# Optimization experiments

Measured on AMD Instinct MI355X. Metric: run time of the kernel, lower is better.

Reference implementation:

```python
import jax, jax.numpy as jnp
import numpy as np

DIM = 1024
SEQ_LEN = 4096
K = 256
HEADS = 16
DIM_HEAD = DIM // HEADS  # 64
BATCH = 4


def setup_inputs() -> dict:
    key = jax.random.key(0)
    ks = jax.random.split(key, 8)
    x = jax.random.normal(ks[0], (BATCH, SEQ_LEN, DIM), dtype=jnp.float32)
    # nn.Linear weights are [out, in]; y = x @ W.T
    std_lin = 1.0 / np.sqrt(DIM)
    Wq = jax.random.uniform(ks[1], (HEADS * DIM_HEAD, DIM), minval=-std_lin, maxval=std_lin, dtype=jnp.float32)
    Wk = jax.random.uniform(ks[2], (HEADS * DIM_HEAD, DIM), minval=-std_lin, maxval=std_lin, dtype=jnp.float32)
    Wv = jax.random.uniform(ks[3], (HEADS * DIM_HEAD, DIM), minval=-std_lin, maxval=std_lin, dtype=jnp.float32)
    # proj_k/proj_v init_: uniform(-1/sqrt(k), 1/sqrt(k)) on [seq_len, k]
    std_p = 1.0 / np.sqrt(K)
    proj_k = jax.random.uniform(ks[4], (SEQ_LEN, K), minval=-std_p, maxval=std_p, dtype=jnp.float32)
    proj_v = jax.random.uniform(ks[5], (SEQ_LEN, K), minval=-std_p, maxval=std_p, dtype=jnp.float32)
    std_o = 1.0 / np.sqrt(HEADS * DIM_HEAD)
    Wo = jax.random.uniform(ks[6], (DIM, HEADS * DIM_HEAD), minval=-std_o, maxval=std_o, dtype=jnp.float32)
    bo = jax.random.uniform(ks[7], (DIM,), minval=-std_o, maxval=std_o, dtype=jnp.float32)
    return {"x": x, "Wq": Wq, "Wk": Wk, "Wv": Wv, "proj_k": proj_k, "proj_v": proj_v, "Wo": Wo, "bo": bo}


def reference(x, Wq, Wk, Wv, proj_k, proj_v, Wo, bo):
    b, n, d = x.shape
    h, dh, k = HEADS, DIM_HEAD, K
    # q/k/v projections
    q = jnp.einsum('bnd,ed->bne', x, Wq)            # [b, n, h*dh]
    keys = jnp.einsum('bnd,ed->bne', x, Wk)         # [b, n, h*dh]
    vals = jnp.einsum('bnd,ed->bne', x, Wv)         # [b, n, h*dh]
    # low-rank projection along sequence: [b, n, e] x [n, k] -> [b, k, e]
    keys = jnp.einsum('bne,nk->bke', keys, proj_k[:n])
    vals = jnp.einsum('bne,nk->bke', vals, proj_v[:n])
    # split heads
    q = q.reshape(b, n, h, dh).transpose(0, 2, 1, 3)        # [b, h, n, dh]
    keys = keys.reshape(b, k, h, dh).transpose(0, 2, 1, 3)  # [b, h, k, dh]
    vals = vals.reshape(b, k, h, dh).transpose(0, 2, 1, 3)  # [b, h, k, dh]
    dots = jnp.einsum('bhnd,bhkd->bhnk', q, keys) * (dh ** -0.5)
    attn = jax.nn.softmax(dots, axis=-1)
    out = jnp.einsum('bhnk,bhkd->bhnd', attn, vals)
    out = out.transpose(0, 2, 1, 3).reshape(b, n, h * dh)
    return jnp.einsum('bne,oe->bno', out, Wo) + bo
```

## Files before the change

kernel.cpp:

```cpp
#include <hip/hip_runtime.h>
#include <hip/hip_bf16.h>
#include <stdint.h>

typedef unsigned short u16;
typedef __attribute__((ext_vector_type(8))) short bf16x8;
typedef __attribute__((ext_vector_type(4))) float f32x4;

#define DEV __device__ __forceinline__

DEV u16 f2bf(float f) {
  union { float f; unsigned u; } v; v.f = f;
  unsigned r = (v.u + 0x7fffu + ((v.u >> 16) & 1u)) >> 16;
  return (u16)r;
}

DEV unsigned pk2(float lo, float hi) {
  union { __hip_bfloat162 h; unsigned u; } c;
  c.h = __float22bfloat162_rn(make_float2(lo, hi));
  return c.u;
}

DEV f32x4 mfma16(bf16x8 a, bf16x8 b, f32x4 c) {
  return __builtin_amdgcn_mfma_f32_16x16x32_bf16(a, b, c, 0, 0, 0);
}

DEV void gload_lds16(const u16* g, u16* l) {
  __builtin_amdgcn_global_load_lds((const __attribute__((address_space(1))) void*)g,
                                   (__attribute__((address_space(3))) void*)l, 16, 0, 0);
}

#define QSCALE 0.18033688011112042f

__global__ void cvt_xpose_kernel(const float* __restrict__ src, u16* __restrict__ dst_rm,
                                 u16* __restrict__ dst_tp, int R, int C,
                                 long zS, long zRM, long zTP) {
  __shared__ u16 tile[64][72];
  src += (size_t)blockIdx.z * zS;
  dst_tp += (size_t)blockIdx.z * zTP;
  int r0 = blockIdx.y * 64, c0 = blockIdx.x * 64;
  int tr = threadIdx.x >> 2, tc = (threadIdx.x & 3) * 16;
  const float* s = src + (size_t)(r0 + tr) * C + c0 + tc;
  u16 loc[16];
#pragma unroll
  for (int q = 0; q < 4; ++q) {
    float4 v = ((const float4*)s)[q];
    loc[q * 4 + 0] = f2bf(v.x); loc[q * 4 + 1] = f2bf(v.y);
    loc[q * 4 + 2] = f2bf(v.z); loc[q * 4 + 3] = f2bf(v.w);
  }
#pragma unroll
  for (int i = 0; i < 16; ++i) tile[tr][tc + i] = loc[i];
  if (dst_rm) {
    u16* d = dst_rm + (size_t)blockIdx.z * zRM + (size_t)(r0 + tr) * C + c0 + tc;
    *(bf16x8*)d = *(const bf16x8*)&loc[0];
    *(bf16x8*)(d + 8) = *(const bf16x8*)&loc[8];
  }
  __syncthreads();
  u16 tmp[16];
#pragma unroll
  for (int i = 0; i < 16; ++i) tmp[i] = tile[tc + i][tr];
  u16* d = dst_tp + (size_t)(c0 + tr) * R + r0 + tc;
  *(bf16x8*)d = *(const bf16x8*)&tmp[0];
  *(bf16x8*)(d + 8) = *(const bf16x8*)&tmp[8];
}

__global__ void cvt_w4_kernel(const float* __restrict__ s0, const float* __restrict__ s1,
                              const float* __restrict__ s2, const float* __restrict__ s3,
                              u16* __restrict__ d0, u16* __restrict__ d1,
                              u16* __restrict__ d2, u16* __restrict__ d3) {
  const float* s; u16* d;
  switch (blockIdx.y) {
    case 0: s = s0; d = d0; break;
    case 1: s = s1; d = d1; break;
    case 2: s = s2; d = d2; break;
    default: s = s3; d = d3; break;
  }
  int i = blockIdx.x * 256 + threadIdx.x;
  float4 v = ((const float4*)s)[i];
  ushort4 o; o.x = f2bf(v.x); o.y = f2bf(v.y); o.z = f2bf(v.z); o.w = f2bf(v.w);
  ((ushort4*)d)[i] = o;
}

__global__ void reduce4_kernel(const float* __restrict__ part, u16* __restrict__ out) {
  int i = blockIdx.x * 256 + threadIdx.x;
  const float4* p = (const float4*)part;
  float4 a = p[i], b = p[i + 524288], c = p[i + 1048576], d = p[i + 1572864];
  ushort4 o;
  o.x = f2bf(a.x + b.x + c.x + d.x);
  o.y = f2bf(a.y + b.y + c.y + d.y);
  o.z = f2bf(a.z + b.z + c.z + d.z);
  o.w = f2bf(a.w + b.w + c.w + d.w);
  ((ushort4*)out)[i] = o;
}

template<int OMODE>
__global__ __launch_bounds__(256, 4)
void gemm_bt_kernel(const u16* __restrict__ A, const u16* __restrict__ Bt,
                    const u16* __restrict__ Bt2, void* __restrict__ Cout,
                    u16* __restrict__ CoutT, const float* __restrict__ bias, float cscale,
                    int ldA, int ldB, int ldC, int Klen,
                    long zA, long zB, long zC, int bMod, long kChunk) {
  __shared__ __align__(16) u16 smA[2][128 * 32];
  __shared__ __align__(16) u16 smB[2][128 * 32];
  const int t = threadIdx.x;
  const int lane = t & 63, wave = t >> 6;
  const int wm = wave & 1, wn = wave >> 1;
  const int g = lane >> 4, r = lane & 15;
  const int id = (blockIdx.y << 3) | blockIdx.x;
  const int s = (id & 7) * gridDim.y + (id >> 3);
  const int bx = s & 7, by = s >> 3;
  const int z = blockIdx.z;
  const int b = z % bMod, kc = z / bMod;
  const u16* Ab = A + (size_t)b * zA + (size_t)kc * kChunk;
  const u16* Bbase = (Bt2 && (b & 1)) ? Bt2 : Bt;
  const u16* Bb = Bbase + (size_t)b * zB + (size_t)kc * kChunk;
  const int m0 = by * 128, n0 = bx * 128;
  const int srow = t >> 2;
  const int lslot = ((t & 3) + 4 - ((srow >> 1) & 3)) & 3;

  f32x4 acc[4][4];
#pragma unroll
  for (int m = 0; m < 4; ++m)
#pragma unroll
    for (int n = 0; n < 4; ++n) acc[m][n] = f32x4{0.f, 0.f, 0.f, 0.f};

  auto STAGE = [&](int buf, int k0) {
#pragma unroll
    for (int p = 0; p < 2; ++p) {
      int row = p * 64 + srow;
      gload_lds16(Ab + (size_t)(m0 + row) * ldA + k0 + lslot * 8, &smA[buf][p * 2048 + wave * 512]);
      gload_lds16(Bb + (size_t)(n0 + row) * ldB + k0 + lslot * 8, &smB[buf][p * 2048 + wave * 512]);
    }
  };

  const int nt = Klen >> 5;
  STAGE(0, 0);
  __syncthreads();
  int cur = 0;
  for (int it = 0; it < nt; ++it) {
    if (it + 1 < nt) STAGE(cur ^ 1, (it + 1) << 5);
    bf16x8 af[4], bfr[4];
#pragma unroll
    for (int m = 0; m < 4; ++m) {
      int row = wm * 64 + m * 16 + r;
      int ps = (g + (row >> 1)) & 3;
      af[m] = *(const bf16x8*)&smA[cur][row * 32 + ps * 8];
    }
#pragma unroll
    for (int n = 0; n < 4; ++n) {
      int row = wn * 64 + n * 16 + r;
      int ps = (g + (row >> 1)) & 3;
      bfr[n] = *(const bf16x8*)&smB[cur][row * 32 + ps * 8];
    }
#pragma unroll
    for (int m = 0; m < 4; ++m)
#pragma unroll
      for (int n = 0; n < 4; ++n)
        acc[m][n] = mfma16(af[m], bfr[n], acc[m][n]);
    __syncthreads();
    cur ^= 1;
  }

  if constexpr (OMODE == 0) {
    u16* C = (u16*)Cout + (size_t)z * zC;
#pragma unroll
    for (int n = 0; n < 4; ++n) {
      int col = n0 + wn * 64 + n * 16 + r;
#pragma unroll
      for (int m = 0; m < 4; ++m) {
        int rowb = m0 + wm * 64 + m * 16 + 4 * g;
#pragma unroll
        for (int rr = 0; rr < 4; ++rr)
          C[(size_t)(rowb + rr) * ldC + col] = f2bf(acc[m][n][rr] * cscale);
      }
    }
  } else if constexpr (OMODE == 3) {
    if ((z & 1) == 0) {
      u16* C = (u16*)Cout + (size_t)(z >> 1) * zC;
#pragma unroll
      for (int n = 0; n < 4; ++n) {
        int col = n0 + wn * 64 + n * 16 + r;
#pragma unroll
        for (int m = 0; m < 4; ++m) {
          int rowb = m0 + wm * 64 + m * 16 + 4 * g;
#pragma unroll
          for (int rr = 0; rr < 4; ++rr)
            C[(size_t)(rowb + rr) * ldC + col] = f2bf(acc[m][n][rr]);
        }
      }
    } else {
      u16* C = CoutT + (size_t)(z >> 1) * zC;
#pragma unroll
      for (int n = 0; n < 4; ++n) {
        int col = n0 + wn * 64 + n * 16 + r;
#pragma unroll
        for (int m = 0; m < 4; ++m) {
          int rowb = m0 + wm * 64 + m * 16 + 4 * g;
          ushort4 o;
          o.x = f2bf(acc[m][n][0]); o.y = f2bf(acc[m][n][1]);
          o.z = f2bf(acc[m][n][2]); o.w = f2bf(acc[m][n][3]);
          *(ushort4*)&C[(size_t)col * 256 + rowb] = o;
        }
      }
    }
  } else {
    float* C = (float*)Cout + (size_t)z * zC;
#pragma unroll
    for (int n = 0; n < 4; ++n) {
      int col = n0 + wn * 64 + n * 16 + r;
      float bv = (OMODE == 1) ? bias[col] : 0.f;
#pragma unroll
      for (int m = 0; m < 4; ++m) {
        int rowb = m0 + wm * 64 + m * 16 + 4 * g;
#pragma unroll
        for (int rr = 0; rr < 4; ++rr)
          C[(size_t)(rowb + rr) * ldC + col] = acc[m][n][rr] + bv;
      }
    }
  }
}

#define MFMA_CLUSTER(MH, NH, AF, BV)                                                    \
  do {                                                                                  \
    __builtin_amdgcn_s_barrier();                                                       \
    __builtin_amdgcn_sched_barrier(0);                                                  \
    __builtin_amdgcn_s_setprio(1);                                                      \
    _Pragma("unroll")                                                                   \
    for (int mi = 0; mi < 4; ++mi)                                                      \
      _Pragma("unroll")                                                                 \
      for (int ni = 0; ni < 2; ++ni) {                                                  \
        acc[(MH)*4+mi][(NH)*2+ni] = mfma16(AF[mi][0], BV[ni][0], acc[(MH)*4+mi][(NH)*2+ni]); \
        acc[(MH)*4+mi][(NH)*2+ni] = mfma16(AF[mi][1], BV[ni][1], acc[(MH)*4+mi][(NH)*2+ni]); \
      }                                                                                 \
    __builtin_amdgcn_s_setprio(0);                                                      \
  } while (0)

#define ENDBAR(W)                                                                       \
  do {                                                                                  \
    if ((W) == 1) asm volatile("s_waitcnt vmcnt(4)" ::: "memory");                      \
    if ((W) == 2) asm volatile("s_waitcnt vmcnt(0)" ::: "memory");                      \
    __builtin_amdgcn_s_barrier();                                                       \
    __builtin_amdgcn_sched_barrier(0);                                                  \
  } while (0)

template<int OMODE>
__global__ __launch_bounds__(512, 1)
void gemm256_kernel(const u16* __restrict__ A, const u16* __restrict__ Bt,
                    void* __restrict__ Cout, const float* __restrict__ bias,
                    float cscale, int ldA, int ldB, int ldC, int Klen) {
  __shared__ __align__(16) u16 lds[65536];
  const int t = threadIdx.x;
  const int lane = t & 63, wave = t >> 6;
  const int g = lane >> 4, r = lane & 15, rm = r & 7;
  const int wm = wave >> 2, wn = wave & 3;
  const int id = blockIdx.y * 4 + blockIdx.x;
  const int sw = (id & 7) * 32 + (id >> 3);
  const int bx = sw & 3, by = sw >> 2;
  const int m0 = by * 256, n0 = bx * 256;

  const int trow = t >> 3, tslot = t & 7;
  const int sslot = tslot ^ (trow & 7);
  const u16* Asrc = A + (size_t)(m0 + trow) * ldA + sslot * 8;
  const u16* Bsrc = Bt + sslot * 8;
  const int bRow0 = n0 + (trow >> 5) * 64 + (trow & 31);
  const int bRow1 = n0 + (2 + (trow >> 5)) * 64 + (trow & 31);

  u16* const A0 = lds;
  u16* const A1 = lds + 16384;
  u16* const B0 = lds + 32768;
  u16* const B1 = lds + 49152;

  auto stageA = [&](u16* buf, int h, int k0) {
    u16* d = buf + h * 8192 + t * 8;
    const u16* s0 = Asrc + (size_t)(h * 64) * ldA + k0;
    gload_lds16(s0, d);
    gload_lds16(s0 + (size_t)128 * ldA, d + 4096);
  };
  auto stageB = [&](u16* buf, int h, int k0) {
    u16* d = buf + h * 8192 + t * 8;
    gload_lds16(Bsrc + (size_t)(bRow0 + h * 32) * ldB + k0, d);
    gload_lds16(Bsrc + (size_t)(bRow1 + h * 32) * ldB + k0, d + 4096);
  };

  const int aoff = wm * 64 + r;
  const int boff = wn * 32 + r;

  auto loadA = [&](bf16x8 af[4][2], const u16* base, int MH) {
#pragma unroll
    for (int mi = 0; mi < 4; ++mi) {
      const u16* rp = base + (MH * 128 + aoff + mi * 16) * 64;
      af[mi][0] = *(const bf16x8*)&rp[(g ^ rm) * 8];
      af[mi][1] = *(const bf16x8*)&rp[((4 + g) ^ rm) * 8];
    }
  };
  auto loadB = [&](bf16x8 bv[2][2], const u16* base, int NH) {
#pragma unroll
    for (int ni = 0; ni < 2; ++ni) {
      const u16* rp = base + (NH * 128 + boff + ni * 16) * 64;
      bv[ni][0] = *(const bf16x8*)&rp[(g ^ rm) * 8];
      bv[ni][1] = *(const bf16x8*)&rp[((4 + g) ^ rm) * 8];
    }
  };

  f32x4 acc[8][4];
#pragma unroll
  for (int m = 0; m < 8; ++m)
#pragma unroll
    for (int n = 0; n < 4; ++n) acc[m][n] = f32x4{0.f, 0.f, 0.f, 0.f};

  stageA(A0, 0, 0); stageB(B0, 0, 0); stageA(A0, 1, 0); stageB(B0, 1, 0);
  stageA(A1, 0, 64); stageB(B1, 0, 64);
  asm volatile("s_waitcnt vmcnt(4)" ::: "memory");
  __builtin_amdgcn_s_barrier();
  __builtin_amdgcn_sched_barrier(0);

  const int nt = Klen >> 6;
  for (int j = 0; j < (nt >> 1); ++j) {
    const int ta = 2 * j, tb = ta + 1;
    const int more = (ta + 2 < nt);
    const int kb = tb * 64, kn = (ta + 2) * 64, kn2 = (tb + 2) * 64;
    bf16x8 af[4][2], bv0[2][2], bv1[2][2];
    loadA(af, A0, 0); loadB(bv0, B0, 0);
    stageA(A1, 1, kb);
    MFMA_CLUSTER(0, 0, af, bv0); ENDBAR(0);
    loadB(bv1, B0, 1);
    stageB(B1, 1, kb);
    MFMA_CLUSTER(0, 1, af, bv1); ENDBAR(0);
    loadA(af, A0, 1);
    if (more) stageA(A0, 0, kn);
    MFMA_CLUSTER(1, 0, af, bv0); ENDBAR(0);
    if (more) stageB(B0, 0, kn);
    MFMA_CLUSTER(1, 1, af, bv1); ENDBAR(more ? 1 : 2);
    loadA(af, A1, 0); loadB(bv0, B1, 0);
    if (more) stageA(A0, 1, kn);
    MFMA_CLUSTER(0, 0, af, bv0); ENDBAR(0);
    loadB(bv1, B1, 1);
    if (more) stageB(B0, 1, kn);
    MFMA_CLUSTER(0, 1, af, bv1); ENDBAR(0);
    loadA(af, A1, 1);
    if (more) stageA(A1, 0, kn2);
    MFMA_CLUSTER(1, 0, af, bv0); ENDBAR(0);
    if (more) stageB(B1, 0, kn2);
    MFMA_CLUSTER(1, 1, af, bv1); ENDBAR(more ? 1 : 2);
  }

  if constexpr (OMODE == 0) {
    u16* myT = lds + wave * 8192;
#pragma unroll
    for (int m = 0; m < 8; ++m)
#pragma unroll
      for (int n = 0; n < 4; ++n)
#pragma unroll
        for (int rr = 0; rr < 4; ++rr) {
          int rl = m * 16 + 4 * g + rr;
          int cl = n * 16 + r;
          myT[rl * 64 + (((cl >> 3) ^ (rl & 7)) << 3) + (cl & 7)] = f2bf(acc[m][n][rr] * cscale);
        }
    u16* Cg = (u16*)Cout + (size_t)(m0 + wm * 128) * ldC + n0 + wn * 64;
#pragma unroll
    for (int i = 0; i < 16; ++i) {
      int idx = i * 64 + lane;
      int row = idx >> 3, c8 = idx & 7;
      bf16x8 v = *(const bf16x8*)&myT[row * 64 + ((c8 ^ (row & 7)) << 3)];
      *(bf16x8*)&Cg[(size_t)row * ldC + c8 * 8] = v;
    }
  } else {
    float* myF = (float*)lds + wave * 4096;
    float bvn[4];
#pragma unroll
    for (int n = 0; n < 4; ++n) bvn[n] = bias[n0 + wn * 64 + n * 16 + r];
    float* Cg = (float*)Cout + (size_t)(m0 + wm * 128) * ldC + n0 + wn * 64;
#pragma unroll
    for (int half = 0; half < 2; ++half) {
#pragma unroll
      for (int m2 = 0; m2 < 4; ++m2)
#pragma unroll
        for (int n = 0; n < 4; ++n)
#pragma unroll
          for (int rr = 0; rr < 4; ++rr) {
            int rl = m2 * 16 + 4 * g + rr;
            int cl = n * 16 + r;
            myF[rl * 64 + (((cl >> 2) ^ (rl & 15)) << 2) + (cl & 3)] =
                acc[half * 4 + m2][n][rr] + bvn[n];
          }
#pragma unroll
      for (int i = 0; i < 16; ++i) {
        int idx = i * 64 + lane;
        int row = idx >> 4, c4 = idx & 15;
        float4 v = *(const float4*)&myF[row * 64 + ((c4 ^ (row & 15)) << 2)];
        *(float4*)&Cg[(size_t)(half * 64 + row) * ldC + c4 * 4] = v;
      }
    }
  }
}

__global__ __launch_bounds__(256, 4)
void attn_kernel(const u16* __restrict__ Q, const u16* __restrict__ Kl,
                 const u16* __restrict__ VT, u16* __restrict__ Out) {
  __shared__ __align__(16) u16 sm[20480];
  const int t = threadIdx.x, lane = t & 63, w = t >> 6;
  const int g = lane >> 4, r = lane & 15;
  const int id = (blockIdx.y << 6) | blockIdx.x;
  const int s = (id & 7) * (gridDim.y << 3) + (id >> 3);
  const int b = blockIdx.z, h = s >> 6, n0 = (s & 63) * 64;
  const u16* Kb = Kl + (size_t)b * 262144 + h * 64;
  const u16* Vb = VT + (size_t)b * 262144 + (size_t)(h * 64) * 256;
  u16* vbase = sm + 16384;

  const int vd = t >> 2;
  const int vsl = (t & 3) ^ (vd & 3);
  auto stage_slice = [&](int kk, int buf) {
    gload_lds16(Vb + (size_t)vd * 256 + kk * 32 + vsl * 8, vbase + buf * 2048 + w * 512);
  };

#pragma unroll
  for (int p = 0; p < 8; ++p) {
    int row = p * 32 + (t >> 3);
    int ls = ((t & 7) + 8 - (row & 7)) & 7;
    gload_lds16(Kb + (size_t)row * 1024 + ls * 8, sm + p * 2048 + w * 512);
  }
  stage_slice(0, 0);
  stage_slice(1, 1);
  const int qrow = n0 + w * 16 + r;
  const u16* Qp = Q + ((size_t)(b * 4096 + qrow)) * 1024 + h * 64 + g * 8;
  bf16x8 aq0 = *(const bf16x8*)Qp;
  bf16x8 aq1 = *(const bf16x8*)(Qp + 32);
  __syncthreads();

  f32x4 dotv[16];
  __builtin_amdgcn_s_setprio(1);
#pragma unroll
  for (int kf = 0; kf < 16; ++kf) {
    int row = kf * 16 + r;
    bf16x8 kb0 = *(const bf16x8*)&sm[row * 64 + ((g + row) & 7) * 8];
    bf16x8 kb1 = *(const bf16x8*)&sm[row * 64 + ((4 + g + row) & 7) * 8];
    f32x4 d = f32x4{0.f, 0.f, 0.f, 0.f};
    d = mfma16(kb0, aq0, d);
    d = mfma16(kb1, aq1, d);
    dotv[kf] = d;
  }
  __builtin_amdgcn_s_setprio(0);
  __syncthreads();

  float mx = -3.4e38f;
#pragma unroll
  for (int kf = 0; kf < 16; ++kf)
    mx = fmaxf(mx, fmaxf(fmaxf(dotv[kf][0], dotv[kf][1]), fmaxf(dotv[kf][2], dotv[kf][3])));
  mx = fmaxf(mx, __shfl_xor(mx, 16, 64));
  mx = fmaxf(mx, __shfl_xor(mx, 32, 64));
  float ssum = 0.f;
#pragma unroll
  for (int kf = 0; kf < 16; ++kf)
#pragma unroll
    for (int j = 0; j < 4; ++j) {
      float p = __builtin_amdgcn_exp2f(dotv[kf][j] - mx);
      dotv[kf][j] = p;
      ssum += p;
    }
  ssum += __shfl_xor(ssum, 16, 64);
  ssum += __shfl_xor(ssum, 32, 64);
  const float inv = 1.f / ssum;
  float invv[4];
#pragma unroll
  for (int rr = 0; rr < 4; ++rr) invv[rr] = __shfl(inv, 4 * g + rr, 64);

  const int q16 = w * 16 + r;
  const int qx = (q16 & 7) << 3;
#pragma unroll
  for (int kf = 0; kf < 16; ++kf) {
    uint2 val;
    val.x = pk2(dotv[kf][0], dotv[kf][1]);
    val.y = pk2(dotv[kf][2], dotv[kf][3]);
    *(uint2*)&sm[(q16 * 256 + kf * 16 + 4 * g) ^ qx] = val;
  }

  f32x4 oacc[4];
#pragma unroll
  for (int df = 0; df < 4; ++df) oacc[df] = f32x4{0.f, 0.f, 0.f, 0.f};
#pragma unroll
  for (int kk = 0; kk < 8; ++kk) {
    bf16x8 ap = *(const bf16x8*)&sm[(q16 * 256 + kk * 32 + g * 8) ^ qx];
    const u16* vb = vbase + (kk & 1) * 2048;
    __builtin_amdgcn_s_setprio(1);
#pragma unroll
    for (int df = 0; df < 4; ++df) {
      int d = df * 16 + r;
      bf16x8 bv = *(const bf16x8*)&vb[d * 32 + (g ^ (d & 3)) * 8];
      oacc[df] = mfma16(ap, bv, oacc[df]);
    }
    __builtin_amdgcn_s_setprio(0);
    if (kk < 7) {
      __syncthreads();
      if (kk < 6) stage_slice(kk + 2, kk & 1);
    }
  }

  u16* myO = sm + w * 4096;
#pragma unroll
  for (int df = 0; df < 4; ++df)
#pragma unroll
    for (int rr = 0; rr < 4; ++rr) {
      int row = 4 * g + rr;
      int col = df * 16 + r;
      myO[row * 64 + (((col >> 3) ^ (row & 7)) << 3) + (col & 7)] = f2bf(oacc[df][rr] * invv[rr]);
    }
#pragma unroll
  for (int i = 0; i < 2; ++i) {
    int idx = i * 64 + lane;
    int row = idx >> 3, c8 = idx & 7;
    bf16x8 v = *(const bf16x8*)&myO[row * 64 + ((c8 ^ (row & 7)) << 3)];
    *(bf16x8*)&Out[((size_t)(b * 4096 + n0 + w * 16 + row)) * 1024 + h * 64 + c8 * 8] = v;
  }
}

extern "C" void kernel_launch(void* const* d_in, const int* in_sizes, int n_in,
                              void* d_out, int out_size, void* d_ws, size_t ws_size,
                              hipStream_t stream) {
  const float* x  = (const float*)d_in[0];
  const float* Wq = (const float*)d_in[1];
  const float* Wk = (const float*)d_in[2];
  const float* Wv = (const float*)d_in[3];
  const float* pk = (const float*)d_in[4];
  const float* pv = (const float*)d_in[5];
  const float* Wo = (const float*)d_in[6];
  const float* bo = (const float*)d_in[7];

  u16* ws = (u16*)d_ws;
  u16* xbf   = ws;
  u16* xT    = xbf + 16777216;
  u16* wqb   = xT + 16777216;
  u16* wkb   = wqb + 1048576;
  u16* wvb   = wkb + 1048576;
  u16* wob   = wvb + 1048576;
  u16* projT = wob + 1048576;
  u16* Qb    = projT + 2097152;
  u16* xp    = Qb + 16777216;
  u16* klow  = xp + 2097152;
  u16* vT    = klow + 1048576;
  u16* aout  = xbf;
  float* xp_part = (float*)Qb;

  cvt_xpose_kernel<<<dim3(16, 64, 4), 256, 0, stream>>>(x, xbf, xT, 4096, 1024,
                                                        4194304, 4194304, 4194304);
  cvt_w4_kernel<<<dim3(1024, 4), 256, 0, stream>>>(Wq, Wk, Wv, Wo, wqb, wkb, wvb, wob);
  cvt_xpose_kernel<<<dim3(4, 64, 1), 256, 0, stream>>>(pk, nullptr, projT, 4096, 256, 0, 0, 0);
  cvt_xpose_kernel<<<dim3(4, 64, 1), 256, 0, stream>>>(pv, nullptr, projT + 1048576, 4096, 256, 0, 0, 0);
  gemm_bt_kernel<2><<<dim3(8, 4, 16), 256, 0, stream>>>(
      projT, xT, nullptr, (void*)xp_part, nullptr, nullptr, 1.f,
      4096, 4096, 1024, 1024, 0, 4194304, 524288, 4, 1024);
  reduce4_kernel<<<2048, 256, 0, stream>>>(xp_part, xp);
  gemm_bt_kernel<3><<<dim3(8, 2, 8), 256, 0, stream>>>(
      xp, wkb, wvb, (void*)klow, vT, nullptr, 1.f,
      1024, 1024, 1024, 1024, 262144, 0, 262144, 8, 0);
  gemm256_kernel<0><<<dim3(4, 64), 512, 0, stream>>>(
      xbf, wqb, (void*)Qb, nullptr, QSCALE, 1024, 1024, 1024, 1024);
  attn_kernel<<<dim3(64, 16, 4), 256, 0, stream>>>(Qb, klow, vT, aout);
  gemm256_kernel<1><<<dim3(4, 64), 512, 0, stream>>>(
      aout, wob, d_out, bo, 1.f, 1024, 1024, 1024, 1024);
}
```

Baseline: 211.7 us.

## Batch-merge projT×xT GEMM, add LDS-staged coalesced fp32 split-K output, trim barriers

```diff
diff --git a/kernel.cpp b/kernel.cpp
--- a/kernel.cpp
+++ b/kernel.cpp
@@ -98,21 +98,22 @@
                     const u16* __restrict__ Bt2, void* __restrict__ Cout,
                     u16* __restrict__ CoutT, const float* __restrict__ bias, float cscale,
                     int ldA, int ldB, int ldC, int Klen,
-                    long zA, long zB, long zC, int bMod, long kChunk) {
+                    long zA, long zB, long zC, int bMod, long kChunkA, long kChunkB) {
   __shared__ __align__(16) u16 smA[2][128 * 32];
   __shared__ __align__(16) u16 smB[2][128 * 32];
   const int t = threadIdx.x;
   const int lane = t & 63, wave = t >> 6;
   const int wm = wave & 1, wn = wave >> 1;
   const int g = lane >> 4, r = lane & 15;
-  const int id = (blockIdx.y << 3) | blockIdx.x;
-  const int s = (id & 7) * gridDim.y + (id >> 3);
-  const int bx = s & 7, by = s >> 3;
+  const int id = blockIdx.y * gridDim.x + blockIdx.x;
+  const int cpx = (gridDim.x * gridDim.y) >> 3;
+  const int s = (id & 7) * cpx + (id >> 3);
+  const int bx = s % gridDim.x, by = s / gridDim.x;
   const int z = blockIdx.z;
   const int b = z % bMod, kc = z / bMod;
-  const u16* Ab = A + (size_t)b * zA + (size_t)kc * kChunk;
+  const u16* Ab = A + (size_t)b * zA + (size_t)kc * kChunkA;
   const u16* Bbase = (Bt2 && (b & 1)) ? Bt2 : Bt;
-  const u16* Bb = Bbase + (size_t)b * zB + (size_t)kc * kChunk;
+  const u16* Bb = Bbase + (size_t)b * zB + (size_t)kc * kChunkB;
   const int m0 = by * 128, n0 = bx * 128;
   const int srow = t >> 2;
   const int lslot = ((t & 3) + 4 - ((srow >> 1) & 3)) & 3;
@@ -172,6 +173,32 @@
         for (int rr = 0; rr < 4; ++rr)
           C[(size_t)(rowb + rr) * ldC + col] = f2bf(acc[m][n][rr] * cscale);
       }
+    }
+  } else if constexpr (OMODE == 2) {
+    float* myF = ((float*)(wave < 2 ? (void*)&smA[0][0] : (void*)&smB[0][0])) + (wave & 1) * 2048;
+    float* Cg = (float*)Cout + (size_t)z * zC + (size_t)(m0 + wm * 64) * ldC + n0 + wn * 64;
+#pragma unroll
+    for (int np = 0; np < 2; ++np) {
+#pragma unroll
+      for (int n2 = 0; n2 < 2; ++n2)
+#pragma unroll
+        for (int m = 0; m < 4; ++m)
+#pragma unroll
+          for (int rr = 0; rr < 4; ++rr) {
+            int rl = m * 16 + 4 * g + rr;
+            int cl = n2 * 16 + r;
+            myF[rl * 32 + ((((cl >> 2) ^ (rl & 7)) & 7) << 2) + (cl & 3)] =
+                acc[m][np * 2 + n2][rr];
+          }
+      __syncthreads();
+#pragma unroll
+      for (int i = 0; i < 8; ++i) {
+        int idx = i * 64 + lane;
+        int row = idx >> 3, c = idx & 7;
+        float4 v = *(const float4*)&myF[row * 32 + (((c ^ (row & 7)) & 7) << 2)];
+        *(float4*)&Cg[(size_t)row * ldC + np * 32 + c * 4] = v;
+      }
+      __syncthreads();
     }
   } else if constexpr (OMODE == 3) {
     if ((z & 1) == 0) {
@@ -221,8 +248,6 @@
 
 #define MFMA_CLUSTER(MH, NH, AF, BV)                                                    \
   do {                                                                                  \
-    __builtin_amdgcn_s_barrier();                                                       \
-    __builtin_amdgcn_sched_barrier(0);                                                  \
     __builtin_amdgcn_s_setprio(1);                                                      \
     _Pragma("unroll")                                                                   \
     for (int mi = 0; mi < 4; ++mi)                                                      \
@@ -239,7 +264,6 @@
     if ((W) == 1) asm volatile("s_waitcnt vmcnt(4)" ::: "memory");                      \
     if ((W) == 2) asm volatile("s_waitcnt vmcnt(0)" ::: "memory");                      \
     __builtin_amdgcn_s_barrier();                                                       \
-    __builtin_amdgcn_sched_barrier(0);                                                  \
   } while (0)
 
 template<int OMODE>
@@ -311,7 +335,6 @@
   stageA(A1, 0, 64); stageB(B1, 0, 64);
   asm volatile("s_waitcnt vmcnt(4)" ::: "memory");
   __builtin_amdgcn_s_barrier();
-  __builtin_amdgcn_sched_barrier(0);
 
   const int nt = Klen >> 6;
   for (int j = 0; j < (nt >> 1); ++j) {
@@ -544,13 +567,13 @@
   cvt_w4_kernel<<<dim3(1024, 4), 256, 0, stream>>>(Wq, Wk, Wv, Wo, wqb, wkb, wvb, wob);
   cvt_xpose_kernel<<<dim3(4, 64, 1), 256, 0, stream>>>(pk, nullptr, projT, 4096, 256, 0, 0, 0);
   cvt_xpose_kernel<<<dim3(4, 64, 1), 256, 0, stream>>>(pv, nullptr, projT + 1048576, 4096, 256, 0, 0, 0);
-  gemm_bt_kernel<2><<<dim3(8, 4, 16), 256, 0, stream>>>(
+  gemm_bt_kernel<2><<<dim3(32, 4, 4), 256, 0, stream>>>(
       projT, xT, nullptr, (void*)xp_part, nullptr, nullptr, 1.f,
-      4096, 4096, 1024, 1024, 0, 4194304, 524288, 4, 1024);
+      4096, 4096, 4096, 1024, 0, 0, 2097152, 1, 1024, 1024);
   reduce4_kernel<<<2048, 256, 0, stream>>>(xp_part, xp);
   gemm_bt_kernel<3><<<dim3(8, 2, 8), 256, 0, stream>>>(
       xp, wkb, wvb, (void*)klow, vT, nullptr, 1.f,
-      1024, 1024, 1024, 1024, 262144, 0, 262144, 8, 0);
+      4096, 1024, 1024, 1024, 1048576, 0, 262144, 2, 1024, 0);
   gemm256_kernel<0><<<dim3(4, 64), 512, 0, stream>>>(
       xbf, wqb, (void*)Qb, nullptr, QSCALE, 1024, 1024, 1024, 1024);
   attn_kernel<<<dim3(64, 16, 4), 256, 0, stream>>>(Qb, klow, vT, aout);
```

Measured after the change: 211.2 us. No clear change (-0.2%).
